# Performance work log

Hardware: AMD Instinct MI355X
Metric: run time of the kernel (lower is better)

The kernel has to match this reference:

```python
import jax, jax.numpy as jnp
import numpy as np

B, S, V = 2, 4096, 50265
L, DM, DFF = 2, 768, 3072
H, D, W = 12, 64, 256  # heads, head_dim, one-sided window (attention_window=512)
NEG = -1e9


def _ln(x, s, b, eps=1e-5):
    m = x.mean(-1, keepdims=True)
    v = ((x - m) ** 2).mean(-1, keepdims=True)
    return (x - m) * jax.lax.rsqrt(v + eps) * s + b


def _heads(y):  # [B,S,DM] -> [B,H,S,D]
    return y.reshape(B, S, H, D).transpose(0, 2, 1, 3)


def _longformer_layer(x, am, p):
    nb = S // W  # number of query blocks
    scale = 1.0 / jnp.sqrt(jnp.asarray(D, x.dtype))
    q = _heads(x @ p['Wq'] + p['bq']) * scale
    k = _heads(x @ p['Wk'] + p['bk'])
    v = _heads(x @ p['Wv'] + p['bv'])
    # overlapping key blocks: block n covers padded positions [n*W, n*W+3W)
    idx = jnp.arange(nb)[:, None] * W + jnp.arange(3 * W)[None, :]  # [nb,3W]
    kp = jnp.pad(k, ((0, 0), (0, 0), (W, W), (0, 0)))
    vp = jnp.pad(v, ((0, 0), (0, 0), (W, W), (0, 0)))
    kb = kp[:, :, idx]  # [B,H,nb,3W,D]
    vb = vp[:, :, idx]
    qb = q.reshape(B, H, nb, W, D)
    scores = jnp.einsum('bhnqd,bhnkd->bhnqk', qb, kb)  # [B,H,nb,W,3W]
    # band mask: query i attends keys within +-W
    qi = jnp.arange(W)[:, None]
    kj = jnp.arange(3 * W)[None, :]
    band = (kj >= qi) & (kj <= qi + 2 * W)  # [W,3W]
    kpos = idx - W  # global key positions, [nb,3W]
    valid = (kpos >= 0) & (kpos < S) & (kpos != 0)  # exclude global tok 0 from band
    amk = jnp.pad(am, ((0, 0), (W, W)))[:, idx] > 0  # [B,nb,3W]
    mask = band[None, None, None] & valid[None, None, :, None, :] & amk[:, None, :, None, :]
    scores = jnp.where(mask, scores, NEG).reshape(B, H, S, 3 * W)
    # global-key column: every query attends token 0 (regular K/V)
    sg = jnp.einsum('bhsd,bhd->bhs', q, k[:, :, 0])
    sg = jnp.where(am[:, None, 0:1] > 0, sg, NEG)
    attn = jax.nn.softmax(jnp.concatenate([scores, sg[..., None]], -1), axis=-1)
    a_band = attn[..., :3 * W].reshape(B, H, nb, W, 3 * W)
    out = jnp.einsum('bhnqk,bhnkd->bhnqd', a_band, vb).reshape(B, H, S, D)
    out = out + attn[..., 3 * W][..., None] * v[:, :, 0][:, :, None, :]
    # global query row (token 0): full attention with dedicated global projections
    qg = ((x[:, 0] @ p['Wqg'] + p['bqg']).reshape(B, H, D)) * scale
    kg = _heads(x @ p['Wkg'] + p['bkg'])
    vg = _heads(x @ p['Wvg'] + p['bvg'])
    sgl = jnp.einsum('bhd,bhsd->bhs', qg, kg)
    sgl = jnp.where(am[:, None, :] > 0, sgl, NEG)
    og = jnp.einsum('bhs,bhsd->bhd', jax.nn.softmax(sgl, axis=-1), vg)
    out = out.at[:, :, 0, :].set(og)
    attn_out = out.transpose(0, 2, 1, 3).reshape(B, S, DM) @ p['Wo'] + p['bo']
    x = _ln(x + attn_out, p['ln1_s'], p['ln1_b'])
    h = jax.nn.gelu(x @ p['W1'] + p['b1']) @ p['W2'] + p['b2']
    return _ln(x + h, p['ln2_s'], p['ln2_b'])


def setup_inputs() -> dict:
    key = jax.random.key(0)
    ks = iter(jax.random.split(key, 40))
    f = lambda *s: jax.random.normal(next(ks), s, jnp.float32) * 0.02
    inp = {
        'input_ids': jax.random.randint(next(ks), (B, S), 0, V),
        'attention_mask': jnp.ones((B, S), jnp.int32),
        'word_emb': f(V, DM), 'pos_emb': f(S, DM),
        'ln_e_s': jnp.ones((DM,)), 'ln_e_b': jnp.zeros((DM,)),
        'Wq': f(L, DM, DM), 'bq': jnp.zeros((L, DM)),
        'Wk': f(L, DM, DM), 'bk': jnp.zeros((L, DM)),
        'Wv': f(L, DM, DM), 'bv': jnp.zeros((L, DM)),
        'Wqg': f(L, DM, DM), 'bqg': jnp.zeros((L, DM)),
        'Wkg': f(L, DM, DM), 'bkg': jnp.zeros((L, DM)),
        'Wvg': f(L, DM, DM), 'bvg': jnp.zeros((L, DM)),
        'Wo': f(L, DM, DM), 'bo': jnp.zeros((L, DM)),
        'ln1_s': jnp.ones((L, DM)), 'ln1_b': jnp.zeros((L, DM)),
        'W1': f(L, DM, DFF), 'b1': jnp.zeros((L, DFF)),
        'W2': f(L, DFF, DM), 'b2': jnp.zeros((L, DM)),
        'ln2_s': jnp.ones((L, DM)), 'ln2_b': jnp.zeros((L, DM)),
        'Wcls': f(DM, 2), 'bcls': jnp.zeros((2,)),
    }
    return inp


def reference(input_ids, attention_mask, word_emb, pos_emb, ln_e_s, ln_e_b,
              Wq, bq, Wk, bk, Wv, bv, Wqg, bqg, Wkg, bkg, Wvg, bvg, Wo, bo,
              ln1_s, ln1_b, W1, b1, W2, b2, ln2_s, ln2_b, Wcls, bcls):
    x = word_emb[input_ids] + pos_emb[None]
    x = _ln(x, ln_e_s, ln_e_b)
    for l in range(L):
        p = dict(Wq=Wq[l], bq=bq[l], Wk=Wk[l], bk=bk[l], Wv=Wv[l], bv=bv[l],
                 Wqg=Wqg[l], bqg=bqg[l], Wkg=Wkg[l], bkg=bkg[l], Wvg=Wvg[l], bvg=bvg[l],
                 Wo=Wo[l], bo=bo[l], ln1_s=ln1_s[l], ln1_b=ln1_b[l],
                 W1=W1[l], b1=b1[l], W2=W2[l], b2=b2[l], ln2_s=ln2_s[l], ln2_b=ln2_b[l])
        x = _longformer_layer(x, attention_mask, p)
    return x[:, 0] @ Wcls + bcls  # logits [B, num_labels]
```

## Files before the change

### kernel.cpp

```cpp
#include <hip/hip_runtime.h>
#include <hip/hip_bf16.h>

#define B_   2
#define S_   4096
#define DM_  768
#define H_   12
#define D_   64
#define W_   256
#define NB_  16
#define DFF_ 3072
#define L_   2
#define QS_  3840
#define NEG_ (-1.0e9f)
#define GC_  16
#define QB_  64
#define NCH_ 18

typedef long long ll;
typedef unsigned short u16;
typedef unsigned int   u32;

typedef __attribute__((ext_vector_type(8))) short bfrag;
typedef __attribute__((ext_vector_type(4))) float ffrag;
typedef __attribute__((address_space(1))) unsigned gu32;
typedef __attribute__((address_space(3))) unsigned lu32;

__device__ __forceinline__ float b2f(u16 u){ union{u32 i; float f;} x; x.i = ((u32)u)<<16; return x.f; }
__device__ __forceinline__ u16 f2b(float f){
  __hip_bfloat16 h = __float2bfloat16(f);
  union{__hip_bfloat16 h; u16 u;} x; x.h = h; return x.u;
}
__device__ __forceinline__ void unp8(uint4 u, float* f){
  union{u32 i; float v;} a;
  a.i = u.x<<16; f[0]=a.v; a.i = u.x&0xffff0000u; f[1]=a.v;
  a.i = u.y<<16; f[2]=a.v; a.i = u.y&0xffff0000u; f[3]=a.v;
  a.i = u.z<<16; f[4]=a.v; a.i = u.z&0xffff0000u; f[5]=a.v;
  a.i = u.w<<16; f[6]=a.v; a.i = u.w&0xffff0000u; f[7]=a.v;
}
__device__ __forceinline__ void gld16(const void* g, void* l){
  __builtin_amdgcn_global_load_lds((gu32*)g, (lu32*)l, 16, 0, 0);
}
__device__ __forceinline__ float bsum256(float v, float* s4){
  #pragma unroll
  for(int o=32;o>0;o>>=1) v += __shfl_down(v,o,64);
  int w = threadIdx.x>>6;
  __syncthreads();
  if((threadIdx.x&63)==0) s4[w]=v;
  __syncthreads();
  return s4[0]+s4[1]+s4[2]+s4[3];
}
__device__ __forceinline__ float bmax256(float v, float* s4){
  #pragma unroll
  for(int o=32;o>0;o>>=1) v = fmaxf(v,__shfl_down(v,o,64));
  int w = threadIdx.x>>6;
  __syncthreads();
  if((threadIdx.x&63)==0) s4[w]=v;
  __syncthreads();
  return fmaxf(fmaxf(s4[0],s4[1]),fmaxf(s4[2],s4[3]));
}
__device__ __forceinline__ float gelu_f(float x){
  return 0.5f*x*(1.0f+tanhf(0.7978845608028654f*(x+0.044715f*x*x*x)));
}

__global__ void k_detect(const void* les, int* flag){
  unsigned u = *(const unsigned*)les;
  *flag = (u == 0x3F803F80u) ? 1 : 0;
}

__global__ void k_cvt(const void* __restrict__ src, ll soff, float* __restrict__ dst, int n, const int* flag){
  int f = *flag;
  int i = blockIdx.x*256 + threadIdx.x;
  int st = gridDim.x*256;
  if(f){
    const u16* s = (const u16*)src + soff;
    for(; i<n; i+=st) dst[i] = b2f(s[i]);
  } else {
    const float* s = (const float*)src + soff;
    for(; i<n; i+=st) dst[i] = s[i];
  }
}

struct CvtArgs { const void* src[32]; float* dst[32]; int soff[32]; int n[32]; };
__global__ void k_cvts(CvtArgs a, const int* __restrict__ flag){
  int seg = blockIdx.y;
  int i = blockIdx.x*256 + threadIdx.x;
  if(i >= a.n[seg]) return;
  int f = *flag;
  float v = f ? b2f(((const u16*)a.src[seg])[a.soff[seg]+i])
              : ((const float*)a.src[seg])[a.soff[seg]+i];
  a.dst[seg][i] = v;
}

__global__ __launch_bounds__(256) void k_tw(const void* __restrict__ src, ll soff, u16* __restrict__ dst,
    int R, int C, const int* __restrict__ flag){
  __shared__ float tile[32][33];
  int f = *flag;
  int tx = threadIdx.x & 31, ty = threadIdx.x >> 5;
  int c = blockIdx.x*32 + tx;
  #pragma unroll
  for(int i=0;i<4;i++){
    int r = blockIdx.y*32 + ty + i*8;
    float v;
    if(f) v = b2f(((const u16*)src)[soff + (ll)r*C + c]);
    else  v = ((const float*)src)[soff + (ll)r*C + c];
    tile[ty + i*8][tx] = v;
  }
  __syncthreads();
  #pragma unroll
  for(int i=0;i<4;i++){
    int orow = blockIdx.x*32 + ty + i*8;
    int oc   = blockIdx.y*32 + tx;
    dst[(ll)orow*R + oc] = f2b(tile[tx][ty + i*8]);
  }
}

struct TwArgs { const void* src[14]; ll soff[14]; u16* dst[14]; };
__global__ __launch_bounds__(256) void k_tws(TwArgs a, const int* __restrict__ flag){
  __shared__ float tile[32][33];
  int z = blockIdx.z;
  const void* src = a.src[z]; ll soff = a.soff[z]; u16* dst = a.dst[z];
  int f = *flag;
  int tx = threadIdx.x & 31, ty = threadIdx.x >> 5;
  int c = blockIdx.x*32 + tx;
  #pragma unroll
  for(int i=0;i<4;i++){
    int r = blockIdx.y*32 + ty + i*8;
    float v;
    if(f) v = b2f(((const u16*)src)[soff + (ll)r*DM_ + c]);
    else  v = ((const float*)src)[soff + (ll)r*DM_ + c];
    tile[ty + i*8][tx] = v;
  }
  __syncthreads();
  #pragma unroll
  for(int i=0;i<4;i++){
    int orow = blockIdx.x*32 + ty + i*8;
    int oc   = blockIdx.y*32 + tx;
    dst[(ll)orow*DM_ + oc] = f2b(tile[tx][ty + i*8]);
  }
}

__global__ __launch_bounds__(256) void k_embed(const int* __restrict__ ids, const void* __restrict__ wemb,
    const float* __restrict__ pos, const float* __restrict__ es, const float* __restrict__ eb,
    float* __restrict__ x, u16* __restrict__ xb, const int* flag){
  __shared__ float s4[4];
  int tok = blockIdx.x;
  int s = tok & (S_-1);
  int t = threadIdx.x;
  int id = ids[tok];
  int f = *flag;
  float v[3];
  #pragma unroll
  for(int j=0;j<3;j++){
    int i = t + j*256;
    float we = f ? b2f(((const u16*)wemb)[(ll)id*DM_ + i])
                 : ((const float*)wemb)[(ll)id*DM_ + i];
    v[j] = we + pos[s*DM_ + i];
  }
  float mean = bsum256(v[0]+v[1]+v[2], s4) * (1.0f/DM_);
  float d0=v[0]-mean, d1=v[1]-mean, d2=v[2]-mean;
  float var = bsum256(d0*d0+d1*d1+d2*d2, s4) * (1.0f/DM_);
  float r = rsqrtf(var + 1e-5f);
  #pragma unroll
  for(int j=0;j<3;j++){
    int i = t + j*256;
    float o = (v[j]-mean)*r*es[i] + eb[i];
    x[(ll)tok*DM_ + i] = o;
    xb[(ll)tok*DM_ + i] = f2b(o);
  }
}

__global__ __launch_bounds__(256) void k_rln(float* __restrict__ x, const float* __restrict__ add,
    const float* __restrict__ sc, const float* __restrict__ bi, u16* __restrict__ xb){
  __shared__ float s4[4];
  int tok = blockIdx.x;
  int t = threadIdx.x;
  float v[3];
  #pragma unroll
  for(int j=0;j<3;j++){
    int i = t + j*256;
    v[j] = x[(ll)tok*DM_+i] + add[(ll)tok*DM_+i];
  }
  float mean = bsum256(v[0]+v[1]+v[2], s4) * (1.0f/DM_);
  float d0=v[0]-mean, d1=v[1]-mean, d2=v[2]-mean;
  float var = bsum256(d0*d0+d1*d1+d2*d2, s4) * (1.0f/DM_);
  float r = rsqrtf(var + 1e-5f);
  #pragma unroll
  for(int j=0;j<3;j++){
    int i = t + j*256;
    float o = (v[j]-mean)*r*sc[i] + bi[i];
    x[(ll)tok*DM_+i] = o;
    xb[(ll)tok*DM_+i] = f2b(o);
  }
}

template<int MODE>
__global__ __launch_bounds__(256) void k_mm(const u16* __restrict__ A, const u16* __restrict__ Bt,
    const float* __restrict__ bias, void* __restrict__ Cout, int M, int N, int K){
  __shared__ __align__(16) u16 As[128*32];
  __shared__ __align__(16) u16 Bs[128*32];
  int tid = threadIdx.x, wave = tid>>6, lane = tid&63;
  int m0 = blockIdx.y*128, n0 = blockIdx.x*128;
  int wm = (wave>>1)*64, wn = (wave&1)*64;
  ffrag acc[4][4];
  #pragma unroll
  for(int i=0;i<4;i++)
    #pragma unroll
    for(int j=0;j<4;j++) acc[i][j] = (ffrag){0.f,0.f,0.f,0.f};
  int lrow = lane>>2, lseg = (lane&3)*8;
  const u16* Ap0 = A  + (ll)(m0 + wave*32 + lrow)*K + lseg;
  const u16* Bp0 = Bt + (ll)(n0 + wave*32 + lrow)*K + lseg;
  u16* AsW0 = As + (wave*2+0)*512;
  u16* AsW1 = As + (wave*2+1)*512;
  u16* BsW0 = Bs + (wave*2+0)*512;
  u16* BsW1 = Bs + (wave*2+1)*512;
  int lane15 = lane&15, quad = lane>>4;
  const u16* ArA = As + (wm + lane15)*32 + quad*8;
  const u16* BrB = Bs + (wn + lane15)*32 + quad*8;
  for(int k0=0; k0<K; k0+=32){
    __syncthreads();
    gld16(Ap0 + k0,             AsW0);
    gld16(Ap0 + k0 + (ll)16*K,  AsW1);
    gld16(Bp0 + k0,             BsW0);
    gld16(Bp0 + k0 + (ll)16*K,  BsW1);
    __syncthreads();
    bfrag af[4], bf[4];
    #pragma unroll
    for(int i=0;i<4;i++) af[i] = *(const bfrag*)(ArA + i*512);
    #pragma unroll
    for(int i=0;i<4;i++) bf[i] = *(const bfrag*)(BrB + i*512);
    #pragma unroll
    for(int i=0;i<4;i++)
      #pragma unroll
      for(int j=0;j<4;j++)
        acc[i][j] = __builtin_amdgcn_mfma_f32_16x16x32_bf16(af[i], bf[j], acc[i][j], 0, 0, 0);
  }
  #pragma unroll
  for(int mi=0;mi<4;mi++){
    #pragma unroll
    for(int ni=0;ni<4;ni++){
      int col = n0 + wn + ni*16 + lane15;
      float bv = bias[col];
      #pragma unroll
      for(int r=0;r<4;r++){
        int row = m0 + wm + mi*16 + quad*4 + r;
        float c = acc[mi][ni][r] + bv;
        if(MODE==2) c = gelu_f(c);
        if(MODE==1) ((float*)Cout)[(ll)row*N + col] = c;
        else        ((u16*)Cout)[(ll)row*N + col] = f2b(c);
      }
    }
  }
}

__global__ __launch_bounds__(256) void k_qg(const float* __restrict__ x, const u16* __restrict__ Wt,
    const float* __restrict__ bg, float* __restrict__ qg){
  int b = blockIdx.y;
  int nn = blockIdx.x*256 + threadIdx.x;
  __shared__ float xs[DM_];
  int t = threadIdx.x;
  #pragma unroll
  for(int j=0;j<3;j++) xs[t + j*256] = x[(ll)(b*S_)*DM_ + t + j*256];
  __syncthreads();
  const uint4* wr = (const uint4*)(Wt + (ll)nn*DM_);
  float acc = bg[nn];
  #pragma unroll 4
  for(int g=0; g<96; g++){
    float tf[8]; unp8(wr[g], tf);
    #pragma unroll
    for(int e=0;e<8;e++) acc = fmaf(xs[g*8+e], tf[e], acc);
  }
  qg[b*DM_ + nn] = acc;
}

__global__ __launch_bounds__(256) void k_band(const u16* __restrict__ qb, const u16* __restrict__ kb,
    const u16* __restrict__ vb, const int* __restrict__ am, u16* __restrict__ aout){
  int nq = blockIdx.x, h = blockIdx.y, b = blockIdx.z;
  int q0 = nq*QB_;
  int tid = threadIdx.x;
  int wave = tid>>6, lane = tid&63, lane15 = lane&15, quad = lane>>4;
  int wq = wave*16;
  __shared__ __align__(16) u16 Ks[32*72];
  __shared__ __align__(16) u16 Vt[64*40];
  __shared__ __align__(16) u16 Ps[4][16*40];
  __shared__ float k0f[64];
  __shared__ float v0f[64];
  __shared__ float cok[32];
  const int kbase = q0 - W_;
  const int am0 = am[b*S_];
  bfrag aq[2];
  {
    const u16* qbase = qb + ((ll)(b*S_ + q0 + wq + lane15))*QS_ + h*64 + quad*8;
    aq[0] = *(const bfrag*)(qbase);
    aq[1] = *(const bfrag*)(qbase + 32);
  }
  if(tid < 64){
    k0f[tid] = b2f(kb[(ll)(b*S_)*QS_ + h*64 + tid]);
    v0f[tid] = b2f(vb[(ll)(b*S_)*QS_ + h*64 + tid]);
  }
  ffrag ao[4];
  #pragma unroll
  for(int j=0;j<4;j++) ao[j] = (ffrag){0.f,0.f,0.f,0.f};
  float ms[4], ls[4];
  #pragma unroll
  for(int i=0;i<4;i++){ ms[i] = -INFINITY; ls[i] = 0.f; }

  #pragma unroll 1
  for(int c=0;c<NCH_;c++){
    __syncthreads();
    {
      int key = tid>>3, seg = tid&7;
      int kp = kbase + c*32 + key;
      uint4 kvec = make_uint4(0,0,0,0);
      if((unsigned)kp < (unsigned)S_)
        kvec = *(const uint4*)(kb + ((ll)(b*S_+kp))*QS_ + h*64 + seg*8);
      *(uint4*)&Ks[key*72 + seg*8] = kvec;
      int kpv = kbase + c*32 + wave*8;
      union { u16 s[8]; uint4 v; } vu;
      #pragma unroll
      for(int j=0;j<8;j++){
        int kp2 = kpv + j;
        vu.s[j] = ((unsigned)kp2 < (unsigned)S_) ? vb[((ll)(b*S_+kp2))*QS_ + h*64 + lane] : (u16)0;
      }
      *(uint4*)&Vt[lane*40 + wave*8] = vu.v;
      if(tid < 32){
        int kp2 = kbase + c*32 + tid;
        cok[tid] = ((kp2>=1) && (kp2<S_) && (am[b*S_+kp2]>0)) ? 0.f : NEG_;
      }
    }
    __syncthreads();
    ffrag as_[2];
    as_[0] = (ffrag){0.f,0.f,0.f,0.f};
    as_[1] = (ffrag){0.f,0.f,0.f,0.f};
    #pragma unroll
    for(int ni=0;ni<2;ni++){
      #pragma unroll
      for(int kc=0;kc<2;kc++){
        bfrag bk = *(const bfrag*)&Ks[(ni*16+lane15)*72 + kc*32 + quad*8];
        as_[ni] = __builtin_amdgcn_mfma_f32_16x16x32_bf16(aq[kc], bk, as_[ni], 0, 0, 0);
      }
    }
    float c0 = cok[lane15], c1 = cok[16+lane15];
    int jg0 = c*32 + lane15, jg1 = jg0 + 16;
    #pragma unroll
    for(int reg=0;reg<4;reg++){
      int qloc = wq + quad*4 + reg;
      float s0 = ((unsigned)(jg0 - qloc) <= 512u) ? as_[0][reg]*0.125f + c0 : NEG_;
      float s1 = ((unsigned)(jg1 - qloc) <= 512u) ? as_[1][reg]*0.125f + c1 : NEG_;
      float cm = fmaxf(s0, s1);
      cm = fmaxf(cm, __shfl_xor(cm,1));
      cm = fmaxf(cm, __shfl_xor(cm,2));
      cm = fmaxf(cm, __shfl_xor(cm,4));
      cm = fmaxf(cm, __shfl_xor(cm,8));
      float mn = fmaxf(ms[reg], cm);
      float al = __expf(ms[reg] - mn);
      float p0 = __expf(s0 - mn), p1 = __expf(s1 - mn);
      float rs = p0 + p1;
      rs += __shfl_xor(rs,1); rs += __shfl_xor(rs,2);
      rs += __shfl_xor(rs,4); rs += __shfl_xor(rs,8);
      ls[reg] = ls[reg]*al + rs;
      ms[reg] = mn;
      #pragma unroll
      for(int nt=0;nt<4;nt++) ao[nt][reg] *= al;
      int prow = quad*4 + reg;
      Ps[wave][prow*40 + (lane15 ^ (quad*8))]        = f2b(p0);
      Ps[wave][prow*40 + ((16 + lane15) ^ (quad*8))] = f2b(p1);
    }
    bfrag bv[4];
    #pragma unroll
    for(int nt=0;nt<4;nt++) bv[nt] = *(const bfrag*)&Vt[(nt*16+lane15)*40 + quad*8];
    int rperm = ((lane15>>2)&3)*8;
    bfrag ap = *(const bfrag*)&Ps[wave][lane15*40 + ((quad*8) ^ rperm)];
    #pragma unroll
    for(int nt=0;nt<4;nt++)
      ao[nt] = __builtin_amdgcn_mfma_f32_16x16x32_bf16(ap, bv[nt], ao[nt], 0, 0, 0);
  }
  float k0v[16];
  #pragma unroll
  for(int kc=0;kc<2;kc++)
    #pragma unroll
    for(int j=0;j<8;j++) k0v[kc*8+j] = k0f[kc*32 + quad*8 + j];
  float cokg = (am0>0) ? 0.f : NEG_;
  float sgm;
  {
    float d = 0.f;
    #pragma unroll
    for(int kc=0;kc<2;kc++)
      #pragma unroll
      for(int j=0;j<8;j++)
        d = fmaf(b2f((u16)aq[kc][j]), k0v[kc*8+j], d);
    d += __shfl_xor(d,16);
    d += __shfl_xor(d,32);
    sgm = d*0.125f + cokg;
  }
  float v0v[4];
  #pragma unroll
  for(int nt=0;nt<4;nt++) v0v[nt] = v0f[nt*16 + lane15];
  #pragma unroll
  for(int reg=0;reg<4;reg++){
    float sg = __shfl(sgm, (quad<<4) + quad*4 + reg);
    float mn = fmaxf(ms[reg], sg);
    float al = __expf(ms[reg] - mn);
    float pg = __expf(sg - mn);
    float inv = 1.f / (ls[reg]*al + pg);
    #pragma unroll
    for(int nt=0;nt<4;nt++)
      ao[nt][reg] = (ao[nt][reg]*al + pg*v0v[nt]) * inv;
  }
  u16* obase = aout + ((ll)(b*S_ + q0 + wq + quad*4))*DM_ + h*64 + lane15;
  #pragma unroll
  for(int reg=0;reg<4;reg++)
    #pragma unroll
    for(int nt=0;nt<4;nt++)
      obase[(ll)reg*DM_ + nt*16] = f2b(ao[nt][reg]);
}

__global__ __launch_bounds__(256) void k_gattn1(const float* __restrict__ qg, const u16* __restrict__ kg,
    const u16* __restrict__ vg, const int* __restrict__ am, float* __restrict__ part){
  int ck = blockIdx.x, h = blockIdx.y, b = blockIdx.z;
  int t = threadIdx.x;
  __shared__ float s4[4];
  __shared__ float qgs[64];
  __shared__ float ps[256];
  __shared__ float obuf[4][64];
  if(t < 64) qgs[t] = qg[b*DM_ + h*64 + t];
  __syncthreads();
  int s = ck*256 + t;
  const uint4* kr = (const uint4*)(kg + (ll)(b*S_+s)*QS_ + h*64);
  float d = 0.f;
  #pragma unroll
  for(int g=0; g<8; g++){
    float tf[8]; unp8(kr[g], tf);
    #pragma unroll
    for(int e=0;e<8;e++) d = fmaf(qgs[g*8+e], tf[e], d);
  }
  float sc = (am[b*S_+s] > 0) ? d*0.125f : NEG_;
  float m_c = bmax256(sc, s4);
  float p = __expf(sc - m_c);
  float l_c = bsum256(p, s4);
  ps[t] = p;
  __syncthreads();
  int dd = t & 63, grp = t >> 6;
  float acc = 0.f;
  const u16* vbase = vg + (ll)(b*S_ + ck*256 + grp*64)*QS_ + h*64 + dd;
  #pragma unroll 8
  for(int j=0;j<64;j++)
    acc = fmaf(ps[grp*64+j], b2f(vbase[(ll)j*QS_]), acc);
  obuf[grp][dd] = acc;
  __syncthreads();
  if(t < 64){
    float o = obuf[0][t] + obuf[1][t] + obuf[2][t] + obuf[3][t];
    float* pp = part + ((ll)(b*H_+h)*GC_ + ck)*66;
    if(t == 0){ pp[0] = m_c; pp[1] = l_c; }
    pp[2+t] = o;
  }
}

__global__ void k_gattn2(const float* __restrict__ part, u16* __restrict__ aout){
  int h = blockIdx.x, b = blockIdx.y;
  int t = threadIdx.x;
  const float* pp = part + ((ll)(b*H_+h)*GC_)*66;
  float m = -INFINITY;
  #pragma unroll
  for(int c=0;c<GC_;c++) m = fmaxf(m, pp[c*66]);
  float l = 0.f, o = 0.f;
  #pragma unroll
  for(int c=0;c<GC_;c++){
    float w = __expf(pp[c*66] - m);
    l += pp[c*66+1]*w;
    o += pp[c*66+2+t]*w;
  }
  aout[(ll)(b*S_)*DM_ + h*64 + t] = f2b(o/l);
}

__global__ __launch_bounds__(256) void k_cls(const float* __restrict__ x, const float* __restrict__ Wc,
    const float* __restrict__ bc, void* out, const int* flag){
  __shared__ float s4[4];
  int t = threadIdx.x;
  float a00=0,a01=0,a10=0,a11=0;
  for(int k=t;k<DM_;k+=256){
    float w0 = Wc[k*2], w1 = Wc[k*2+1];
    float x0 = x[k];
    float x1 = x[(ll)S_*DM_ + k];
    a00 = fmaf(x0,w0,a00); a01 = fmaf(x0,w1,a01);
    a10 = fmaf(x1,w0,a10); a11 = fmaf(x1,w1,a11);
  }
  float r00 = bsum256(a00,s4);
  float r01 = bsum256(a01,s4);
  float r10 = bsum256(a10,s4);
  float r11 = bsum256(a11,s4);
  if(t==0){
    float o[4] = {r00+bc[0], r01+bc[1], r10+bc[0], r11+bc[1]};
    if(*flag){
      __hip_bfloat16* ob = (__hip_bfloat16*)out;
      for(int i=0;i<4;i++) ob[i] = __float2bfloat16(o[i]);
    } else {
      float* of = (float*)out;
      for(int i=0;i<4;i++) of[i] = o[i];
    }
  }
}

extern "C" void kernel_launch(void* const* d_in, const int* in_sizes, int n_in,
                              void* d_out, int out_size, void* d_ws, size_t ws_size,
                              hipStream_t stream){
  char* wsb = (char*)d_ws;
  size_t off = 0;
  auto alloc = [&](size_t bytes)->size_t{ off = (off + 255) & ~(size_t)255; size_t r = off; off += bytes; return r; };
  const size_t TOK = (size_t)B_*S_;
  size_t P_flag = alloc(16);
  size_t P_pos  = alloc((size_t)S_*DM_*4);
  size_t P_les  = alloc(DM_*4), P_leb = alloc(DM_*4);
  size_t P_bqkv = alloc((size_t)L_*QS_*4);
  size_t P_bqg  = alloc((size_t)L_*DM_*4);
  size_t P_bo   = alloc((size_t)L_*DM_*4);
  size_t P_b1   = alloc((size_t)L_*DFF_*4);
  size_t P_b2   = alloc((size_t)L_*DM_*4);
  size_t P_l1s  = alloc((size_t)L_*DM_*4), P_l1b = alloc((size_t)L_*DM_*4);
  size_t P_l2s  = alloc((size_t)L_*DM_*4), P_l2b = alloc((size_t)L_*DM_*4);
  size_t P_Wc   = alloc(DM_*2*4), P_bc = alloc(64);
  size_t P_qgb  = alloc((size_t)B_*DM_*4);
  size_t P_part = alloc((size_t)B_*H_*GC_*66*4);
  size_t P_Wqkvt= alloc((size_t)L_*QS_*DM_*2);
  size_t P_Wqgt = alloc((size_t)L_*DM_*DM_*2);
  size_t P_Wot  = alloc((size_t)L_*DM_*DM_*2);
  size_t P_W1t  = alloc((size_t)L_*DM_*DFF_*2);
  size_t P_W2t  = alloc((size_t)L_*DFF_*DM_*2);
  size_t P_x    = alloc(TOK*DM_*4);
  size_t P_tmp  = alloc(TOK*DM_*4);
  size_t P_xb   = alloc(TOK*DM_*2);
  size_t P_qkv  = alloc(TOK*QS_*2);
  size_t P_aout = alloc(TOK*DM_*2);
  size_t P_h    = alloc(TOK*DFF_*2);

  int* flag = (int*)(wsb + P_flag);
  #define FP(o) ((float*)(wsb + (o)))
  #define HP(o) ((u16*)(wsb + (o)))

  k_detect<<<1,1,0,stream>>>(d_in[4], flag);

  k_cvt<<<2048,256,0,stream>>>(d_in[3], 0, FP(P_pos), S_*DM_, flag);

  {
    CvtArgs ca{};
    int ns = 0;
    auto addcv = [&](int idx, size_t dstoff, int soff, int nelem){
      ca.src[ns] = d_in[idx]; ca.dst[ns] = FP(dstoff); ca.soff[ns] = soff; ca.n[ns] = nelem; ns++;
    };
    addcv(4, P_les, 0, DM_); addcv(5, P_leb, 0, DM_);
    addcv(28, P_Wc, 0, DM_*2); addcv(29, P_bc, 0, 2);
    const int bidx[5] = {7,9,11,15,17};
    for(int l=0;l<L_;l++){
      for(int s=0;s<5;s++) addcv(bidx[s], P_bqkv + ((size_t)l*QS_ + s*DM_)*4, l*DM_, DM_);
      addcv(13, P_bqg + (size_t)l*DM_*4,  l*DM_,  DM_);
      addcv(19, P_bo  + (size_t)l*DM_*4,  l*DM_,  DM_);
      addcv(23, P_b1  + (size_t)l*DFF_*4, l*DFF_, DFF_);
      addcv(25, P_b2  + (size_t)l*DM_*4,  l*DM_,  DM_);
      addcv(20, P_l1s + (size_t)l*DM_*4,  l*DM_,  DM_);
      addcv(21, P_l1b + (size_t)l*DM_*4,  l*DM_,  DM_);
      addcv(26, P_l2s + (size_t)l*DM_*4,  l*DM_,  DM_);
      addcv(27, P_l2b + (size_t)l*DM_*4,  l*DM_,  DM_);
    }
    for(int s2=ns; s2<32; s2++){ ca.src[s2]=d_in[4]; ca.dst[s2]=FP(P_les); ca.soff[s2]=0; ca.n[s2]=0; }
    k_cvts<<<dim3(12, ns),256,0,stream>>>(ca, flag);
  }

  {
    TwArgs ta{};
    int nt_ = 0;
    const int widx[5] = {6,8,10,14,16};
    for(int l=0;l<L_;l++){
      for(int s=0;s<5;s++){
        ta.src[nt_] = d_in[widx[s]]; ta.soff[nt_] = (ll)l*DM_*DM_;
        ta.dst[nt_] = HP(P_Wqkvt) + (size_t)l*QS_*DM_ + (size_t)s*DM_*DM_; nt_++;
      }
      ta.src[nt_] = d_in[12]; ta.soff[nt_] = (ll)l*DM_*DM_;
      ta.dst[nt_] = HP(P_Wqgt) + (size_t)l*DM_*DM_; nt_++;
      ta.src[nt_] = d_in[18]; ta.soff[nt_] = (ll)l*DM_*DM_;
      ta.dst[nt_] = HP(P_Wot) + (size_t)l*DM_*DM_; nt_++;
    }
    k_tws<<<dim3(24,24,14),256,0,stream>>>(ta, flag);
  }
  for(int l=0;l<L_;l++){
    k_tw<<<dim3(DFF_/32, DM_/32),256,0,stream>>>(d_in[22], (ll)l*DM_*DFF_,
        HP(P_W1t) + (size_t)l*DFF_*DM_, DM_, DFF_, flag);
    k_tw<<<dim3(DM_/32, DFF_/32),256,0,stream>>>(d_in[24], (ll)l*DFF_*DM_,
        HP(P_W2t) + (size_t)l*DM_*DFF_, DFF_, DM_, flag);
  }

  const int* am = (const int*)d_in[1];
  k_embed<<<(int)TOK,256,0,stream>>>((const int*)d_in[0], d_in[2], FP(P_pos), FP(P_les), FP(P_leb),
                                     FP(P_x), HP(P_xb), flag);
  for(int l=0;l<L_;l++){
    const u16* Wqkvt_l = HP(P_Wqkvt) + (size_t)l*QS_*DM_;
    k_mm<0><<<dim3(QS_/128, TOK/128),256,0,stream>>>(HP(P_xb), Wqkvt_l, FP(P_bqkv) + (size_t)l*QS_,
        HP(P_qkv), (int)TOK, QS_, DM_);
    k_qg<<<dim3(3,B_),256,0,stream>>>(FP(P_x), HP(P_Wqgt) + (size_t)l*DM_*DM_, FP(P_bqg) + (size_t)l*DM_, FP(P_qgb));
    k_band<<<dim3(S_/QB_,H_,B_),256,0,stream>>>(HP(P_qkv), HP(P_qkv)+DM_, HP(P_qkv)+2*DM_, am, HP(P_aout));
    k_gattn1<<<dim3(GC_,H_,B_),256,0,stream>>>(FP(P_qgb), HP(P_qkv)+3*DM_, HP(P_qkv)+4*DM_, am, FP(P_part));
    k_gattn2<<<dim3(H_,B_),64,0,stream>>>(FP(P_part), HP(P_aout));
    k_mm<1><<<dim3(DM_/128, TOK/128),256,0,stream>>>(HP(P_aout), HP(P_Wot) + (size_t)l*DM_*DM_,
        FP(P_bo) + (size_t)l*DM_, FP(P_tmp), (int)TOK, DM_, DM_);
    k_rln<<<(int)TOK,256,0,stream>>>(FP(P_x), FP(P_tmp), FP(P_l1s) + (size_t)l*DM_, FP(P_l1b) + (size_t)l*DM_, HP(P_xb));
    k_mm<2><<<dim3(DFF_/128, TOK/128),256,0,stream>>>(HP(P_xb), HP(P_W1t) + (size_t)l*DFF_*DM_,
        FP(P_b1) + (size_t)l*DFF_, HP(P_h), (int)TOK, DFF_, DM_);
    k_mm<1><<<dim3(DM_/128, TOK/128),256,0,stream>>>(HP(P_h), HP(P_W2t) + (size_t)l*DM_*DFF_,
        FP(P_b2) + (size_t)l*DM_, FP(P_tmp), (int)TOK, DM_, DFF_);
    k_rln<<<(int)TOK,256,0,stream>>>(FP(P_x), FP(P_tmp), FP(P_l2s) + (size_t)l*DM_, FP(P_l2b) + (size_t)l*DM_, HP(P_xb));
  }
  k_cls<<<1,256,0,stream>>>(FP(P_x), FP(P_Wc), FP(P_bc), d_out, flag);
}
```

Measured before the change: 1.140 ms.

## Transpose band-attention MFMA layout, prefetch K/V to registers, skip out-of-range chunks

Reworks the sliding-window attention kernel. The score MFMA is computed transposed (K as A operand, Q as B), so each lane owns one query row. Softmax max and sum then need only two cross-lane shuffles, and the P tile and output are written as packed vectors. The next chunk's K/V is fetched into registers before the current chunk's compute, and the key-mask column is precomputed once per block. Chunks lying entirely outside the sequence are skipped at edge blocks. The cost is higher register pressure from the prefetch buffers, plus some risk from the changed P-tile layout and the chunk-bound arithmetic.

Result: faster. 1.048 ms (-8.0%).

```diff
diff --git a/kernel.cpp b/kernel.cpp
--- a/kernel.cpp
+++ b/kernel.cpp
@@ -282,106 +282,127 @@
   __shared__ __align__(16) u16 Ks[32*72];
   __shared__ __align__(16) u16 Vt[64*40];
   __shared__ __align__(16) u16 Ps[4][16*40];
-  __shared__ float k0f[64];
-  __shared__ float v0f[64];
-  __shared__ float cok[32];
+  __shared__ __align__(16) float cokA[QB_+2*W_];
+  __shared__ __align__(16) float k0f[64];
+  __shared__ __align__(16) float v0f[64];
   const int kbase = q0 - W_;
   const int am0 = am[b*S_];
+  for(int i=tid; i<QB_+2*W_; i+=256){
+    int kp = kbase + i;
+    cokA[i] = ((kp>=1) && (kp<S_) && (am[b*S_+kp]>0)) ? 0.f : NEG_;
+  }
+  if(tid < 64){
+    k0f[tid] = b2f(kb[(ll)(b*S_)*QS_ + h*64 + tid]);
+    v0f[tid] = b2f(vb[(ll)(b*S_)*QS_ + h*64 + tid]);
+  }
   bfrag aq[2];
   {
     const u16* qbase = qb + ((ll)(b*S_ + q0 + wq + lane15))*QS_ + h*64 + quad*8;
     aq[0] = *(const bfrag*)(qbase);
     aq[1] = *(const bfrag*)(qbase + 32);
   }
-  if(tid < 64){
-    k0f[tid] = b2f(kb[(ll)(b*S_)*QS_ + h*64 + tid]);
-    v0f[tid] = b2f(vb[(ll)(b*S_)*QS_ + h*64 + tid]);
-  }
   ffrag ao[4];
   #pragma unroll
   for(int j=0;j<4;j++) ao[j] = (ffrag){0.f,0.f,0.f,0.f};
-  float ms[4], ls[4];
-  #pragma unroll
-  for(int i=0;i<4;i++){ ms[i] = -INFINITY; ls[i] = 0.f; }
-
-  #pragma unroll 1
-  for(int c=0;c<NCH_;c++){
-    __syncthreads();
-    {
-      int key = tid>>3, seg = tid&7;
-      int kp = kbase + c*32 + key;
-      uint4 kvec = make_uint4(0,0,0,0);
+  float ms = -INFINITY, ls = 0.f;
+
+  int c_lo = (kbase < 1) ? ((1 - kbase) / 32) : 0;
+  if(c_lo < 0) c_lo = 0;
+  int c_hi = (S_ - 1 - kbase) / 32 + 1;
+  if(c_hi > NCH_) c_hi = NCH_;
+
+  int skey = tid>>3, sseg = tid&7;
+  uint4 kreg;
+  union { u16 s[8]; uint4 v; } vreg;
+  auto FETCH = [&](int c){
+    int kp0 = kbase + c*32;
+    if(kp0 >= 0 && kp0 + 31 < S_){
+      kreg = *(const uint4*)(kb + ((ll)(b*S_ + kp0 + skey))*QS_ + h*64 + sseg*8);
+      const u16* vp = vb + ((ll)(b*S_ + kp0 + wave*8))*QS_ + h*64 + lane;
+      #pragma unroll
+      for(int j=0;j<8;j++) vreg.s[j] = vp[(ll)j*QS_];
+    } else {
+      int kp = kp0 + skey;
+      kreg = make_uint4(0,0,0,0);
       if((unsigned)kp < (unsigned)S_)
-        kvec = *(const uint4*)(kb + ((ll)(b*S_+kp))*QS_ + h*64 + seg*8);
-      *(uint4*)&Ks[key*72 + seg*8] = kvec;
-      int kpv = kbase + c*32 + wave*8;
-      union { u16 s[8]; uint4 v; } vu;
+        kreg = *(const uint4*)(kb + ((ll)(b*S_+kp))*QS_ + h*64 + sseg*8);
       #pragma unroll
       for(int j=0;j<8;j++){
-        int kp2 = kpv + j;
-        vu.s[j] = ((unsigned)kp2 < (unsigned)S_) ? vb[((ll)(b*S_+kp2))*QS_ + h*64 + lane] : (u16)0;
+        int kp2 = kp0 + wave*8 + j;
+        vreg.s[j] = ((unsigned)kp2 < (unsigned)S_) ? vb[((ll)(b*S_+kp2))*QS_ + h*64 + lane] : (u16)0;
       }
-      *(uint4*)&Vt[lane*40 + wave*8] = vu.v;
-      if(tid < 32){
-        int kp2 = kbase + c*32 + tid;
-        cok[tid] = ((kp2>=1) && (kp2<S_) && (am[b*S_+kp2]>0)) ? 0.f : NEG_;
-      }
-    }
+    }
+  };
+  FETCH(c_lo);
+
+  #pragma unroll 1
+  for(int c=c_lo; c<c_hi; c++){
     __syncthreads();
-    ffrag as_[2];
-    as_[0] = (ffrag){0.f,0.f,0.f,0.f};
-    as_[1] = (ffrag){0.f,0.f,0.f,0.f};
-    #pragma unroll
-    for(int ni=0;ni<2;ni++){
+    *(uint4*)&Ks[skey*72 + sseg*8] = kreg;
+    *(uint4*)&Vt[lane*40 + wave*8] = vreg.v;
+    __syncthreads();
+    if(c+1 < c_hi) FETCH(c+1);
+    ffrag st0 = (ffrag){0.f,0.f,0.f,0.f};
+    ffrag st1 = (ffrag){0.f,0.f,0.f,0.f};
+    #pragma unroll
+    for(int kc=0;kc<2;kc++){
+      bfrag k0r = *(const bfrag*)&Ks[(     lane15)*72 + kc*32 + quad*8];
+      bfrag k1r = *(const bfrag*)&Ks[(16 + lane15)*72 + kc*32 + quad*8];
+      st0 = __builtin_amdgcn_mfma_f32_16x16x32_bf16(k0r, aq[kc], st0, 0, 0, 0);
+      st1 = __builtin_amdgcn_mfma_f32_16x16x32_bf16(k1r, aq[kc], st1, 0, 0, 0);
+    }
+    float4 ck0 = *(const float4*)&cokA[c*32 + quad*4];
+    float4 ck1 = *(const float4*)&cokA[c*32 + 16 + quad*4];
+    float cka[8] = {ck0.x,ck0.y,ck0.z,ck0.w, ck1.x,ck1.y,ck1.z,ck1.w};
+    int qloc = wq + lane15;
+    int jg0 = c*32 + quad*4;
+    float s[8];
+    #pragma unroll
+    for(int r=0;r<4;r++){
+      s[r]   = ((unsigned)(jg0 + r      - qloc) <= 512u) ? st0[r]*0.125f + cka[r]   : NEG_;
+      s[4+r] = ((unsigned)(jg0 + 16 + r - qloc) <= 512u) ? st1[r]*0.125f + cka[4+r] : NEG_;
+    }
+    float cm = s[0];
+    #pragma unroll
+    for(int r=1;r<8;r++) cm = fmaxf(cm, s[r]);
+    cm = fmaxf(cm, __shfl_xor(cm,16));
+    cm = fmaxf(cm, __shfl_xor(cm,32));
+    float mn = fmaxf(ms, cm);
+    float al = __expf(ms - mn);
+    float p[8], rs = 0.f;
+    #pragma unroll
+    for(int r=0;r<8;r++){ p[r] = __expf(s[r] - mn); rs += p[r]; }
+    rs += __shfl_xor(rs,16);
+    rs += __shfl_xor(rs,32);
+    ls = ls*al + rs;
+    ms = mn;
+    #pragma unroll
+    for(int nt=0;nt<4;nt++)
       #pragma unroll
-      for(int kc=0;kc<2;kc++){
-        bfrag bk = *(const bfrag*)&Ks[(ni*16+lane15)*72 + kc*32 + quad*8];
-        as_[ni] = __builtin_amdgcn_mfma_f32_16x16x32_bf16(aq[kc], bk, as_[ni], 0, 0, 0);
-      }
-    }
-    float c0 = cok[lane15], c1 = cok[16+lane15];
-    int jg0 = c*32 + lane15, jg1 = jg0 + 16;
-    #pragma unroll
-    for(int reg=0;reg<4;reg++){
-      int qloc = wq + quad*4 + reg;
-      float s0 = ((unsigned)(jg0 - qloc) <= 512u) ? as_[0][reg]*0.125f + c0 : NEG_;
-      float s1 = ((unsigned)(jg1 - qloc) <= 512u) ? as_[1][reg]*0.125f + c1 : NEG_;
-      float cm = fmaxf(s0, s1);
-      cm = fmaxf(cm, __shfl_xor(cm,1));
-      cm = fmaxf(cm, __shfl_xor(cm,2));
-      cm = fmaxf(cm, __shfl_xor(cm,4));
-      cm = fmaxf(cm, __shfl_xor(cm,8));
-      float mn = fmaxf(ms[reg], cm);
-      float al = __expf(ms[reg] - mn);
-      float p0 = __expf(s0 - mn), p1 = __expf(s1 - mn);
-      float rs = p0 + p1;
-      rs += __shfl_xor(rs,1); rs += __shfl_xor(rs,2);
-      rs += __shfl_xor(rs,4); rs += __shfl_xor(rs,8);
-      ls[reg] = ls[reg]*al + rs;
-      ms[reg] = mn;
-      #pragma unroll
-      for(int nt=0;nt<4;nt++) ao[nt][reg] *= al;
-      int prow = quad*4 + reg;
-      Ps[wave][prow*40 + (lane15 ^ (quad*8))]        = f2b(p0);
-      Ps[wave][prow*40 + ((16 + lane15) ^ (quad*8))] = f2b(p1);
-    }
-    bfrag bv[4];
-    #pragma unroll
-    for(int nt=0;nt<4;nt++) bv[nt] = *(const bfrag*)&Vt[(nt*16+lane15)*40 + quad*8];
-    int rperm = ((lane15>>2)&3)*8;
-    bfrag ap = *(const bfrag*)&Ps[wave][lane15*40 + ((quad*8) ^ rperm)];
-    #pragma unroll
-    for(int nt=0;nt<4;nt++)
-      ao[nt] = __builtin_amdgcn_mfma_f32_16x16x32_bf16(ap, bv[nt], ao[nt], 0, 0, 0);
-  }
-  float k0v[16];
-  #pragma unroll
-  for(int kc=0;kc<2;kc++)
-    #pragma unroll
-    for(int j=0;j<8;j++) k0v[kc*8+j] = k0f[kc*32 + quad*8 + j];
-  float cokg = (am0>0) ? 0.f : NEG_;
+      for(int r=0;r<4;r++) ao[nt][r] *= al;
+    u16 pw[8];
+    #pragma unroll
+    for(int r=0;r<8;r++) pw[r] = f2b(p[r]);
+    uint2 w0, w1;
+    w0.x = (u32)pw[0] | ((u32)pw[1]<<16); w0.y = (u32)pw[2] | ((u32)pw[3]<<16);
+    w1.x = (u32)pw[4] | ((u32)pw[5]<<16); w1.y = (u32)pw[6] | ((u32)pw[7]<<16);
+    *(uint2*)&Ps[wave][lane15*40 + quad*4]      = w0;
+    *(uint2*)&Ps[wave][lane15*40 + 16 + quad*4] = w1;
+    bfrag pf = *(const bfrag*)&Ps[wave][lane15*40 + quad*8];
+    #pragma unroll
+    for(int nt=0;nt<4;nt++){
+      bfrag vf = *(const bfrag*)&Vt[(nt*16+lane15)*40 + quad*8];
+      ao[nt] = __builtin_amdgcn_mfma_f32_16x16x32_bf16(vf, pf, ao[nt], 0, 0, 0);
+    }
+  }
   float sgm;
   {
+    float4 ka0 = *(const float4*)&k0f[quad*8];
+    float4 ka1 = *(const float4*)&k0f[quad*8 + 4];
+    float4 kb0 = *(const float4*)&k0f[32 + quad*8];
+    float4 kb1 = *(const float4*)&k0f[32 + quad*8 + 4];
+    float k0v[16] = {ka0.x,ka0.y,ka0.z,ka0.w, ka1.x,ka1.y,ka1.z,ka1.w,
+                     kb0.x,kb0.y,kb0.z,kb0.w, kb1.x,kb1.y,kb1.z,kb1.w};
     float d = 0.f;
     #pragma unroll
     for(int kc=0;kc<2;kc++)
@@ -390,28 +411,25 @@
         d = fmaf(b2f((u16)aq[kc][j]), k0v[kc*8+j], d);
     d += __shfl_xor(d,16);
     d += __shfl_xor(d,32);
-    sgm = d*0.125f + cokg;
-  }
-  float v0v[4];
-  #pragma unroll
-  for(int nt=0;nt<4;nt++) v0v[nt] = v0f[nt*16 + lane15];
-  #pragma unroll
-  for(int reg=0;reg<4;reg++){
-    float sg = __shfl(sgm, (quad<<4) + quad*4 + reg);
-    float mn = fmaxf(ms[reg], sg);
-    float al = __expf(ms[reg] - mn);
-    float pg = __expf(sg - mn);
-    float inv = 1.f / (ls[reg]*al + pg);
-    #pragma unroll
-    for(int nt=0;nt<4;nt++)
-      ao[nt][reg] = (ao[nt][reg]*al + pg*v0v[nt]) * inv;
-  }
-  u16* obase = aout + ((ll)(b*S_ + q0 + wq + quad*4))*DM_ + h*64 + lane15;
-  #pragma unroll
-  for(int reg=0;reg<4;reg++)
-    #pragma unroll
-    for(int nt=0;nt<4;nt++)
-      obase[(ll)reg*DM_ + nt*16] = f2b(ao[nt][reg]);
+    sgm = d*0.125f + ((am0>0) ? 0.f : NEG_);
+  }
+  float mn = fmaxf(ms, sgm);
+  float al = __expf(ms - mn);
+  float pg = __expf(sgm - mn);
+  float inv = 1.f / (ls*al + pg);
+  u16* obase = aout + ((ll)(b*S_ + q0 + wq + lane15))*DM_ + h*64;
+  #pragma unroll
+  for(int nt=0;nt<4;nt++){
+    float4 v0q = *(const float4*)&v0f[nt*16 + quad*4];
+    float v0a[4] = {v0q.x, v0q.y, v0q.z, v0q.w};
+    u16 o[4];
+    #pragma unroll
+    for(int r=0;r<4;r++) o[r] = f2b((ao[nt][r]*al + pg*v0a[r]) * inv);
+    uint2 w;
+    w.x = (u32)o[0] | ((u32)o[1]<<16);
+    w.y = (u32)o[2] | ((u32)o[3]<<16);
+    *(uint2*)&obase[nt*16 + quad*4] = w;
+  }
 }
 
 __global__ __launch_bounds__(256) void k_gattn1(const float* __restrict__ qg, const u16* __restrict__ kg,
```
